# Performance work log

Hardware: AMD Instinct MI355X
Metric: run time of the kernel (lower is better)

Reference implementation:

```python
import math
import jax, jax.numpy as jnp
import numpy as np

B, C, T, N, H = 4, 512, 2048, 4096, 4


def setup_inputs() -> dict:
    key = jax.random.key(0)
    ks = jax.random.split(key, 6)
    w = lambda k, shape: jax.random.normal(k, shape, dtype=jnp.float32) * 0.02
    return {
        "hidden_states": jax.random.normal(ks[0], (B, C, T), dtype=jnp.float32),
        "codebook_hidden_states": jax.random.normal(ks[1], (N, C), dtype=jnp.float32),
        # Linear weights stored as (in, out) so application is x @ W + b
        "Wq": w(ks[2], (C, C)), "bq": jnp.zeros((C,), jnp.float32),
        "Wk": w(ks[3], (C, C)), "bk": jnp.zeros((C,), jnp.float32),
        "Wv": w(ks[4], (C, C)), "bv": jnp.zeros((C,), jnp.float32),
        "Wp": w(ks[5], (C, H)), "bp": jnp.zeros((H,), jnp.float32),
    }


def reference(hidden_states, codebook_hidden_states, Wq, bq, Wk, bk, Wv, bv, Wp, bp):
    b, c, t = hidden_states.shape
    n = codebook_hidden_states.shape[0]
    h = bp.shape[0]
    d = c // h
    hs = hidden_states.transpose(0, 2, 1)                               # [B,T,C]
    q = (hs @ Wq + bq).reshape(b, t, h, d).transpose(0, 2, 1, 3)        # [B,H,T,d]
    k = (codebook_hidden_states @ Wk + bk).reshape(n, h, d).transpose(1, 0, 2)  # [H,N,d]
    v = codebook_hidden_states @ Wv + bv                                # [N,C]
    cg = hs @ Wp + bp                                                   # [B,T,H] head-pool gates
    scale = 1.0 / math.sqrt(d)
    logits_h = jnp.einsum('bhtd,hnd->bhnt', q, k) * scale               # [B,H,N,T]
    logits = jnp.einsum('bth,bhnt->bnt', cg, logits_h) / math.sqrt(h)   # [B,N,T]
    soft = jax.nn.softmax(logits, axis=1)                               # over codebook axis N
    idx = jnp.argmax(soft, axis=1)                                      # [B,T]
    hard = jax.nn.one_hot(idx, n, dtype=logits.dtype).transpose(0, 2, 1)  # [B,N,T]
    # straight-through: value == hard, gradient flows through soft
    one_hot = soft + jax.lax.stop_gradient(hard - soft)
    z_q = jnp.einsum('bnt,nd->bdt', one_hot, v)                         # [B,C,T]
    return logits, idx[:, None, :], z_q
```

## Files before the change

kernel.cpp:

```cpp
#include <hip/hip_runtime.h>
#include <hip/hip_bf16.h>
#include <cstddef>
#include <cstdint>

#define BB 4
#define CC 512
#define TT 2048
#define NN 4096
#define HH 4

constexpr float KFAC       = 0.04419417382415922f;
constexpr float INV_S18    = 1.0f / 262144.0f;
constexpr float INV_SCALE2 = 1.0f / (512.0f * 512.0f);

typedef _Float16 f16x8 __attribute__((ext_vector_type(8)));
typedef _Float16 f16x4 __attribute__((ext_vector_type(4)));
typedef float    f32x4 __attribute__((ext_vector_type(4)));

__device__ __forceinline__ void gld16(const void* g, void* s) {
    __builtin_amdgcn_global_load_lds(
        (const __attribute__((address_space(1))) void*)g,
        (__attribute__((address_space(3))) void*)s, 16, 0, 0);
}

struct HL { _Float16 h, l; };
__device__ __forceinline__ HL split512(float x) {
    float v = x * 512.0f;
    _Float16 h = (_Float16)v;
    return { h, (_Float16)(v - (float)h) };
}

__global__ __launch_bounds__(256) void k_split(
    const float* __restrict__ src, _Float16* __restrict__ hi, _Float16* __restrict__ lo, int n4)
{
    int q = blockIdx.x * 256 + threadIdx.x;
    if (q >= n4) return;
    float4 v = *(const float4*)(src + (size_t)q * 4);
    f16x4 H, L;
    HL a = split512(v.x); H[0] = a.h; L[0] = a.l;
    HL b = split512(v.y); H[1] = b.h; L[1] = b.l;
    HL c = split512(v.z); H[2] = c.h; L[2] = c.l;
    HL d = split512(v.w); H[3] = d.h; L[3] = d.l;
    *(f16x4*)(hi + (size_t)q * 4) = H;
    *(f16x4*)(lo + (size_t)q * 4) = L;
}

__device__ __forceinline__ void tsplit_body(
    const float* __restrict__ src, _Float16* __restrict__ hi, _Float16* __restrict__ lo,
    int S, int R, int r0, int s0)
{
    __shared__ float ls[64][65];
    const int tid = threadIdx.x;
    #pragma unroll
    for (int i = 0; i < 4; ++i) {
        int q = tid + i * 256;
        int row = q >> 4, c4 = (q & 15) * 4;
        float4 v = *(const float4*)(src + (size_t)(r0 + row) * S + s0 + c4);
        ls[row][c4] = v.x; ls[row][c4 + 1] = v.y;
        ls[row][c4 + 2] = v.z; ls[row][c4 + 3] = v.w;
    }
    __syncthreads();
    #pragma unroll
    for (int i = 0; i < 2; ++i) {
        int q = tid + i * 256;
        int orow = q >> 3, seg = (q & 7) * 8;
        f16x8 H, L;
        #pragma unroll
        for (int j = 0; j < 8; ++j) {
            HL s = split512(ls[seg + j][orow]);
            H[j] = s.h; L[j] = s.l;
        }
        size_t off = (size_t)(s0 + orow) * R + r0 + seg;
        *(f16x8*)(hi + off) = H;
        *(f16x8*)(lo + off) = L;
    }
}

__global__ __launch_bounds__(256) void k_tsplit(
    const float* __restrict__ src, _Float16* __restrict__ hi, _Float16* __restrict__ lo,
    long sbatch, long dbatch, int S, int R)
{
    src += (size_t)blockIdx.z * sbatch;
    hi  += (size_t)blockIdx.z * dbatch;
    lo  += (size_t)blockIdx.z * dbatch;
    tsplit_body(src, hi, lo, S, R, blockIdx.y * 64, blockIdx.x * 64);
}

__global__ __launch_bounds__(256) void k_tsplit_w(
    const float* __restrict__ w0, const float* __restrict__ w1, const float* __restrict__ w2,
    _Float16* __restrict__ h0, _Float16* __restrict__ h1, _Float16* __restrict__ h2,
    _Float16* __restrict__ l0, _Float16* __restrict__ l1, _Float16* __restrict__ l2)
{
    const int z = blockIdx.z;
    const float* src = z == 0 ? w0 : z == 1 ? w1 : w2;
    _Float16* hi = z == 0 ? h0 : z == 1 ? h1 : h2;
    _Float16* lo = z == 0 ? l0 : z == 1 ? l1 : l2;
    tsplit_body(src, hi, lo, CC, CC, blockIdx.y * 64, blockIdx.x * 64);
}

#define MFMA_TILE_DECLS                                                       \
    __shared__ __align__(16) _Float16 Ah[128][32];                            \
    __shared__ __align__(16) _Float16 Al[128][32];                            \
    __shared__ __align__(16) _Float16 Bh[128][32];                            \
    __shared__ __align__(16) _Float16 Bl[128][32];                            \
    const int tid  = threadIdx.x;                                             \
    const int w    = tid >> 6;                                                \
    const int l    = tid & 63;                                                \
    const int quad = l >> 4;                                                  \
    const int l15  = l & 15;                                                  \
    const int wm   = (w >> 1) * 64;                                           \
    const int wn   = (w & 1) * 64;                                            \
    const int rA   = l >> 2;                                                  \
    const int cA   = (l & 3) * 8;                                             \
    f32x4 acc[4][4];                                                          \
    _Pragma("unroll") for (int i = 0; i < 4; ++i)                             \
        _Pragma("unroll") for (int j = 0; j < 4; ++j)                         \
            acc[i][j] = (f32x4){0.f, 0.f, 0.f, 0.f};

#define MFMA_TILE_STAGE(pAh, pAl, pBh, pBl, k0, srcStride)                    \
    gld16(pAh + k0,                    &Ah[w * 32][0]);                       \
    gld16(pAh + k0 + 16 * (srcStride), &Ah[w * 32 + 16][0]);                  \
    gld16(pAl + k0,                    &Al[w * 32][0]);                       \
    gld16(pAl + k0 + 16 * (srcStride), &Al[w * 32 + 16][0]);                  \
    gld16(pBh + k0,                    &Bh[w * 32][0]);                       \
    gld16(pBh + k0 + 16 * (srcStride), &Bh[w * 32 + 16][0]);                  \
    gld16(pBl + k0,                    &Bl[w * 32][0]);                       \
    gld16(pBl + k0 + 16 * (srcStride), &Bl[w * 32 + 16][0]);

#define MFMA_TILE_COMPUTE                                                     \
    {                                                                         \
        f16x8 fah[4], fal[4], fbh[4], fbl[4];                                 \
        _Pragma("unroll") for (int i = 0; i < 4; ++i) {                       \
            fah[i] = *(const f16x8*)&Ah[wm + i * 16 + l15][quad * 8];         \
            fal[i] = *(const f16x8*)&Al[wm + i * 16 + l15][quad * 8];         \
            fbh[i] = *(const f16x8*)&Bh[wn + i * 16 + l15][quad * 8];         \
            fbl[i] = *(const f16x8*)&Bl[wn + i * 16 + l15][quad * 8];         \
        }                                                                     \
        _Pragma("unroll") for (int i = 0; i < 4; ++i)                         \
            _Pragma("unroll") for (int j = 0; j < 4; ++j) {                   \
                acc[i][j] = __builtin_amdgcn_mfma_f32_16x16x32_f16(fah[i], fbh[j], acc[i][j], 0, 0, 0); \
                acc[i][j] = __builtin_amdgcn_mfma_f32_16x16x32_f16(fah[i], fbl[j], acc[i][j], 0, 0, 0); \
                acc[i][j] = __builtin_amdgcn_mfma_f32_16x16x32_f16(fal[i], fbh[j], acc[i][j], 0, 0, 0); \
            }                                                                 \
    }

__global__ __launch_bounds__(256, 2) void k_proj_all(
    const _Float16* __restrict__ hsTh, const _Float16* __restrict__ hsTl,
    const _Float16* __restrict__ cbhi, const _Float16* __restrict__ cblo,
    const _Float16* __restrict__ wqTh, const _Float16* __restrict__ wqTl,
    const _Float16* __restrict__ wkTh, const _Float16* __restrict__ wkTl,
    const _Float16* __restrict__ wvTh, const _Float16* __restrict__ wvTl,
    const float* __restrict__ bq, const float* __restrict__ bk, const float* __restrict__ bv,
    const float* __restrict__ Wp, const float* __restrict__ bp,
    _Float16* __restrict__ qhi, _Float16* __restrict__ qlo,
    _Float16* __restrict__ khi, _Float16* __restrict__ klo, float* __restrict__ vproj)
{
    const int z    = blockIdx.z;
    const int y    = blockIdx.y;
    const int c0   = blockIdx.x * 128;
    const int path = z == 0 ? 0 : (y < 32 ? 1 : 2);
    const int m0   = (z == 0 ? y : (y & 31)) * 128;
    const int hblk = c0 >> 7;

    const _Float16* srcAh = z == 0 ? hsTh : cbhi;
    const _Float16* srcAl = z == 0 ? hsTl : cblo;
    const _Float16* bTh   = path == 0 ? wqTh : path == 1 ? wkTh : wvTh;
    const _Float16* bTl   = path == 0 ? wqTl : path == 1 ? wkTl : wvTl;
    const float*    bias  = path == 0 ? bq   : path == 1 ? bk   : bv;

    MFMA_TILE_DECLS
    __shared__ float wp_sh[32];
    __shared__ float gate_sh[128];
    float gate = 0.f;

    const _Float16* pAh = srcAh + (size_t)(m0 + w * 32 + rA) * CC + cA;
    const _Float16* pAl = srcAl + (size_t)(m0 + w * 32 + rA) * CC + cA;
    const _Float16* pBh = bTh   + (size_t)(c0 + w * 32 + rA) * CC + cA;
    const _Float16* pBl = bTl   + (size_t)(c0 + w * 32 + rA) * CC + cA;

    for (int k0 = 0; k0 < CC; k0 += 32) {
        MFMA_TILE_STAGE(pAh, pAl, pBh, pBl, k0, CC)
        if (path == 0 && tid < 32) wp_sh[tid] = Wp[(size_t)(k0 + tid) * HH + hblk];
        __syncthreads();
        MFMA_TILE_COMPUTE
        if (path == 0 && tid < 128) {
            #pragma unroll
            for (int s = 0; s < 4; ++s) {
                f16x8 hv = *(const f16x8*)&Ah[tid][s * 8];
                f16x8 lv = *(const f16x8*)&Al[tid][s * 8];
                #pragma unroll
                for (int jj = 0; jj < 8; ++jj)
                    gate = fmaf((float)hv[jj] + (float)lv[jj], wp_sh[s * 8 + jj], gate);
            }
        }
        __syncthreads();
    }

    if (path == 0) {
        if (tid < 128)
            gate_sh[tid] = (gate * (1.0f / 512.0f) + bp[hblk]) * KFAC;
        __syncthreads();
        #pragma unroll
        for (int i = 0; i < 4; ++i)
            #pragma unroll
            for (int j = 0; j < 4; ++j) {
                int col = c0 + wn + j * 16 + l15;
                float bi = bias[col];
                #pragma unroll
                for (int r = 0; r < 4; ++r) {
                    int rloc = wm + i * 16 + quad * 4 + r;
                    float v = fmaf(acc[i][j][r], INV_S18, bi) * gate_sh[rloc];
                    HL s = split512(v);
                    qhi[(size_t)(m0 + rloc) * CC + col] = s.h;
                    qlo[(size_t)(m0 + rloc) * CC + col] = s.l;
                }
            }
    } else if (path == 1) {
        #pragma unroll
        for (int i = 0; i < 4; ++i)
            #pragma unroll
            for (int j = 0; j < 4; ++j) {
                int col = c0 + wn + j * 16 + l15;
                float bi = bias[col];
                #pragma unroll
                for (int r = 0; r < 4; ++r) {
                    int row = m0 + wm + i * 16 + quad * 4 + r;
                    float v = fmaf(acc[i][j][r], INV_S18, bi);
                    HL s = split512(v);
                    khi[(size_t)row * CC + col] = s.h;
                    klo[(size_t)row * CC + col] = s.l;
                }
            }
    } else {
        #pragma unroll
        for (int i = 0; i < 4; ++i)
            #pragma unroll
            for (int j = 0; j < 4; ++j) {
                int col = c0 + wn + j * 16 + l15;
                float bi = bias[col];
                #pragma unroll
                for (int r = 0; r < 4; ++r) {
                    int row = m0 + wm + i * 16 + quad * 4 + r;
                    vproj[(size_t)row * CC + col] = fmaf(acc[i][j][r], INV_S18, bi);
                }
            }
    }
}

#define BAR   __builtin_amdgcn_s_barrier()
#define LGKM0 { asm volatile("s_waitcnt lgkmcnt(0)" ::: "memory"); __builtin_amdgcn_sched_barrier(0); }
#define PRIO1 __builtin_amdgcn_s_setprio(1)
#define PRIO0 __builtin_amdgcn_s_setprio(0)

#define STAGE_A(D, KT) {                                                      \
    int sg_ = (KT) >> 3; int kof_ = ((KT) & 7) * 64;                          \
    const _Float16* ab_ = (sg_ == 1 ? klo : khi) + arow0 + kof_;              \
    gld16(ab_ + soff0,         &smem[(D) * 32768 + (w * 2 + 0) * 512]);       \
    gld16(ab_ + soff1,         &smem[(D) * 32768 + (w * 2 + 1) * 512]);       \
    gld16(ab_ + 65536 + soff0, &smem[(D) * 32768 + 8192 + (w * 2 + 0) * 512]);\
    gld16(ab_ + 65536 + soff1, &smem[(D) * 32768 + 8192 + (w * 2 + 1) * 512]);\
}
#define STAGE_B(D, KT) {                                                      \
    int sg_ = (KT) >> 3; int kof_ = ((KT) & 7) * 64;                          \
    const _Float16* bb_ = (sg_ == 2 ? qlo : qhi) + brow0 + kof_;              \
    gld16(bb_ + soff0,         &smem[(D) * 32768 + 16384 + (w * 2 + 0) * 512]);\
    gld16(bb_ + soff1,         &smem[(D) * 32768 + 16384 + (w * 2 + 1) * 512]);\
    gld16(bb_ + 65536 + soff0, &smem[(D) * 32768 + 24576 + (w * 2 + 0) * 512]);\
    gld16(bb_ + 65536 + soff1, &smem[(D) * 32768 + 24576 + (w * 2 + 1) * 512]);\
}
#define RD_A(D, HF) {                                                         \
    _Pragma("unroll") for (int ii = 0; ii < 4; ++ii)                          \
      _Pragma("unroll") for (int kk = 0; kk < 2; ++kk)                        \
        ah[ii][kk] = *(const f16x8*)&smem[(D) * 32768 + ha * 8192 +           \
                         ((HF) * 4 + ii) * 1024 + kk * 32 + rdoffh];          \
}
#define RD_B(D, HF) {                                                         \
    _Pragma("unroll") for (int jj = 0; jj < 2; ++jj)                          \
      _Pragma("unroll") for (int kk = 0; kk < 2; ++kk)                        \
        bf[(HF) * 2 + jj][kk] = *(const f16x8*)&smem[(D) * 32768 + 16384 +    \
            hb * 8192 + wb64f + ((HF) * 2 + jj) * 1024 + kk * 32 + rdoffh];   \
}
#define MM(AH, BH) {                                                          \
    _Pragma("unroll") for (int kk = 0; kk < 2; ++kk)                          \
      _Pragma("unroll") for (int ii = 0; ii < 4; ++ii)                        \
        _Pragma("unroll") for (int jj = 0; jj < 2; ++jj)                      \
          acc[(AH) * 4 + ii][(BH) * 2 + jj] =                                 \
            __builtin_amdgcn_mfma_f32_16x16x32_f16(ah[ii][kk],                \
                bf[(BH) * 2 + jj][kk], acc[(AH) * 4 + ii][(BH) * 2 + jj], 0, 0, 0); \
}
#define KTILE(D, KTN, DOSTAGE) {                                              \
    if (DOSTAGE) STAGE_A(1 - (D), KTN);                                       \
    RD_A(D, 0); RD_B(D, 0);                                                   \
    BAR; LGKM0; PRIO1; MM(0, 0); PRIO0; BAR;                                  \
    if (DOSTAGE) STAGE_B(1 - (D), KTN);                                       \
    RD_B(D, 1);                                                               \
    BAR; LGKM0; PRIO1; MM(0, 1); PRIO0; BAR;                                  \
    RD_A(D, 1);                                                               \
    BAR; LGKM0; PRIO1; MM(1, 1); PRIO0; BAR;                                  \
    PRIO1; MM(1, 0); PRIO0;                                                   \
    if (DOSTAGE) { asm volatile("s_waitcnt vmcnt(0)" ::: "memory"); }         \
    BAR;                                                                      \
}

__global__ __launch_bounds__(512, 2) void k_logits_8p(
    const _Float16* __restrict__ khi, const _Float16* __restrict__ klo,
    const _Float16* __restrict__ qhi, const _Float16* __restrict__ qlo,
    float* __restrict__ logits,
    float* __restrict__ pval,
    int*   __restrict__ pidx)
{
    __shared__ __align__(16) _Float16 smem[65536];

    const int f  = blockIdx.x + 8 * (blockIdx.y + 16 * blockIdx.z);
    const int fs = (f & 7) * 64 + (f >> 3);
    const int t0 = (fs & 7) * 256;
    const int by = (fs >> 3) & 15;
    const int b  = fs >> 7;
    const int n0 = by * 256;

    const int tid  = threadIdx.x;
    const int w    = tid >> 6;
    const int l    = tid & 63;
    const int quad = l >> 4;
    const int l15  = l & 15;
    const int wm   = (w >> 2) * 128;
    const int ha   = w >> 2;
    const int wn   = (w & 3) * 64;
    const int hb   = (w & 3) >> 1;
    const int wb64f = (w & 1) * 4096;

    const size_t arow0 = (size_t)n0 * CC;
    const size_t brow0 = ((size_t)b * TT + t0) * CC;

    size_t soff0, soff1;
    {
        int p0 = (w * 2 + 0) * 64 + l;
        int s0 = p0 ^ (((p0 >> 5) & 1) << 1);
        soff0 = (size_t)(s0 >> 3) * CC + (size_t)(s0 & 7) * 8;
        int p1 = (w * 2 + 1) * 64 + l;
        int s1 = p1 ^ (((p1 >> 5) & 1) << 1);
        soff1 = (size_t)(s1 >> 3) * CC + (size_t)(s1 & 7) * 8;
    }
    const int rdoffh = (l15 * 64 + quad * 8) ^ ((((l15 >> 2) & 1)) << 4);

    f32x4 acc[8][4];
    #pragma unroll
    for (int i = 0; i < 8; ++i)
        #pragma unroll
        for (int j = 0; j < 4; ++j)
            acc[i][j] = (f32x4){0.f, 0.f, 0.f, 0.f};
    f16x8 ah[4][2];
    f16x8 bf[4][2];

    STAGE_A(0, 0); STAGE_B(0, 0);
    asm volatile("s_waitcnt vmcnt(0)" ::: "memory");
    BAR;

    for (int kt2 = 0; kt2 < 12; ++kt2) {
        const int kt = kt2 * 2;
        KTILE(0, kt + 1, 1);
        KTILE(1, kt + 2, kt2 < 11);
    }

    {
        const size_t lb = ((size_t)b * NN + n0 + wm) * TT + t0 + wn;
        #pragma unroll
        for (int i = 0; i < 8; ++i)
            #pragma unroll
            for (int r = 0; r < 4; ++r) {
                const size_t rowoff = lb + (size_t)(i * 16 + quad * 4 + r) * TT;
                #pragma unroll
                for (int j = 0; j < 4; ++j)
                    logits[rowoff + j * 16 + l15] = acc[i][j][r] * INV_SCALE2;
            }
    }
    float bvj[4]; int bnj[4];
    #pragma unroll
    for (int j = 0; j < 4; ++j) {
        float bv = -3.0e38f; int bn = 0;
        #pragma unroll
        for (int i = 0; i < 8; ++i)
            #pragma unroll
            for (int r = 0; r < 4; ++r) {
                float v = acc[i][j][r] * INV_SCALE2;
                int row = n0 + wm + i * 16 + quad * 4 + r;
                if (v > bv) { bv = v; bn = row; }
            }
        #pragma unroll
        for (int m = 16; m <= 32; m <<= 1) {
            float ov = __shfl_xor(bv, m, 64);
            int   on = __shfl_xor(bn, m, 64);
            if (ov > bv || (ov == bv && on < bn)) { bv = ov; bn = on; }
        }
        bvj[j] = bv; bnj[j] = bn;
    }
    float* rv = (float*)smem;
    int*   ri = (int*)(smem + 1024);
    __syncthreads();
    if (w >= 4 && l < 16) {
        #pragma unroll
        for (int j = 0; j < 4; ++j) {
            rv[wn + j * 16 + l] = bvj[j];
            ri[wn + j * 16 + l] = bnj[j];
        }
    }
    __syncthreads();
    if (w < 4 && l < 16) {
        #pragma unroll
        for (int j = 0; j < 4; ++j) {
            int cl = wn + j * 16 + l;
            float bv = bvj[j]; int bn = bnj[j];
            float ov = rv[cl];
            if (ov > bv) { bv = ov; bn = ri[cl]; }
            size_t o = ((size_t)b * 16 + by) * TT + t0 + cl;
            pval[o] = bv;
            pidx[o] = bn;
        }
    }
}

__global__ __launch_bounds__(256) void k_finalize(
    const float* __restrict__ pval,
    const int*   __restrict__ pidx,
    const float* __restrict__ vproj,
    float* __restrict__ idx_out,
    float* __restrict__ zq)
{
    const int b  = blockIdx.y;
    const int t0 = blockIdx.x * 32;
    const int tid = threadIdx.x;

    __shared__ int sfin[32];
    if (tid < 32) {
        const int t = t0 + tid;
        float bv = -3.0e38f; int bn = 0;
        #pragma unroll
        for (int k = 0; k < 16; ++k) {
            size_t o = ((size_t)b * 16 + k) * TT + t;
            float v = pval[o];
            if (v > bv) { bv = v; bn = pidx[o]; }
        }
        idx_out[(size_t)b * TT + t] = (float)bn;
        sfin[tid] = bn;
    }
    __syncthreads();
    for (int pos = tid; pos < 32 * CC; pos += 256) {
        int c = pos >> 5, tl = pos & 31;
        zq[((size_t)b * CC + c) * TT + t0 + tl] = vproj[(size_t)sfin[tl] * CC + c];
    }
}

extern "C" void kernel_launch(void* const* d_in, const int* in_sizes, int n_in,
                              void* d_out, int out_size, void* d_ws, size_t ws_size,
                              hipStream_t stream)
{
    (void)in_sizes; (void)n_in; (void)out_size; (void)ws_size;
    const float* hs = (const float*)d_in[0];
    const float* cb = (const float*)d_in[1];
    const float* Wq = (const float*)d_in[2];
    const float* bq = (const float*)d_in[3];
    const float* Wk = (const float*)d_in[4];
    const float* bk = (const float*)d_in[5];
    const float* Wv = (const float*)d_in[6];
    const float* bv = (const float*)d_in[7];
    const float* Wp = (const float*)d_in[8];
    const float* bp = (const float*)d_in[9];

    char* ws = (char*)d_ws;
    const size_t MB = 1024 * 1024;
    _Float16* hsTh = (_Float16*)(ws);
    _Float16* hsTl = (_Float16*)(ws + 8  * MB);
    _Float16* qhi  = (_Float16*)(ws + 16 * MB);
    _Float16* qlo  = (_Float16*)(ws + 24 * MB);
    _Float16* cbhi = (_Float16*)(ws + 32 * MB);
    _Float16* cblo = (_Float16*)(ws + 36 * MB);
    _Float16* khi  = (_Float16*)(ws + 40 * MB);
    _Float16* klo  = (_Float16*)(ws + 44 * MB);
    float*    vproj= (float*)   (ws + 48 * MB);
    _Float16* wqTh = (_Float16*)(ws + 56 * MB);
    _Float16* wqTl = (_Float16*)(ws + 56 * MB + 524288);
    _Float16* wkTh = (_Float16*)(ws + 57 * MB);
    _Float16* wkTl = (_Float16*)(ws + 57 * MB + 524288);
    _Float16* wvTh = (_Float16*)(ws + 58 * MB);
    _Float16* wvTl = (_Float16*)(ws + 58 * MB + 524288);
    float* pval = (float*)(ws + 32 * MB);
    int*   pidx = (int*)  (ws + 33 * MB);

    float* logits = (float*)d_out;
    float* idxf   = logits + (size_t)BB * NN * TT;
    float* zq     = idxf + (size_t)BB * TT;

    k_split<<<dim3((NN * CC / 4 + 255) / 256), 256, 0, stream>>>(
        cb, cbhi, cblo, NN * CC / 4);
    k_tsplit<<<dim3(TT / 64, CC / 64, BB), 256, 0, stream>>>(
        hs, hsTh, hsTl, (long)CC * TT, (long)TT * CC, TT, CC);
    k_tsplit_w<<<dim3(CC / 64, CC / 64, 3), 256, 0, stream>>>(
        Wq, Wk, Wv, wqTh, wkTh, wvTh, wqTl, wkTl, wvTl);

    k_proj_all<<<dim3(CC / 128, 64, 2), 256, 0, stream>>>(
        hsTh, hsTl, cbhi, cblo,
        wqTh, wqTl, wkTh, wkTl, wvTh, wvTl,
        bq, bk, bv, Wp, bp,
        qhi, qlo, khi, klo, vproj);

    k_logits_8p<<<dim3(TT / 256, NN / 256, BB), 512, 0, stream>>>(
        khi, klo, qhi, qlo, logits, pval, pidx);

    k_finalize<<<dim3(TT / 32, BB), 256, 0, stream>>>(
        pval, pidx, vproj, idxf, zq);
}
```

Measured before the change: 331.5 us.

## Split global-to-LDS staging into half-tiles with partial vmcnt waits

Reworks the software pipeline of the split-fp16 logits GEMM. Each next-tile load is now issued as four half-tile chunks spread across the MFMA phases, and partial vmcnt waits replace the single full drain at the end of each k-tile. The epilogue tile is peeled into its own macro. The LDS swizzle also changes to an XOR on 8-element chunks per row, which alters the read offsets. The goal is to keep more global loads in flight during compute and avoid a full memory stall per tile. The cost is tighter wait counting that must be exactly right for the data to be correct.

```diff
diff --git a/kernel.cpp b/kernel.cpp
--- a/kernel.cpp
+++ b/kernel.cpp
@@ -251,34 +251,42 @@
 #define LGKM0 { asm volatile("s_waitcnt lgkmcnt(0)" ::: "memory"); __builtin_amdgcn_sched_barrier(0); }
 #define PRIO1 __builtin_amdgcn_s_setprio(1)
 #define PRIO0 __builtin_amdgcn_s_setprio(0)
-
-#define STAGE_A(D, KT) {                                                      \
-    int sg_ = (KT) >> 3; int kof_ = ((KT) & 7) * 64;                          \
-    const _Float16* ab_ = (sg_ == 1 ? klo : khi) + arow0 + kof_;              \
-    gld16(ab_ + soff0,         &smem[(D) * 32768 + (w * 2 + 0) * 512]);       \
-    gld16(ab_ + soff1,         &smem[(D) * 32768 + (w * 2 + 1) * 512]);       \
-    gld16(ab_ + 65536 + soff0, &smem[(D) * 32768 + 8192 + (w * 2 + 0) * 512]);\
-    gld16(ab_ + 65536 + soff1, &smem[(D) * 32768 + 8192 + (w * 2 + 1) * 512]);\
-}
-#define STAGE_B(D, KT) {                                                      \
-    int sg_ = (KT) >> 3; int kof_ = ((KT) & 7) * 64;                          \
-    const _Float16* bb_ = (sg_ == 2 ? qlo : qhi) + brow0 + kof_;              \
-    gld16(bb_ + soff0,         &smem[(D) * 32768 + 16384 + (w * 2 + 0) * 512]);\
-    gld16(bb_ + soff1,         &smem[(D) * 32768 + 16384 + (w * 2 + 1) * 512]);\
-    gld16(bb_ + 65536 + soff0, &smem[(D) * 32768 + 24576 + (w * 2 + 0) * 512]);\
-    gld16(bb_ + 65536 + soff1, &smem[(D) * 32768 + 24576 + (w * 2 + 1) * 512]);\
+#define VMW(N) asm volatile("s_waitcnt vmcnt(" #N ")" ::: "memory")
+
+#define ST_A(D, HF, SRC) {                                                    \
+    _Pragma("unroll") for (int qi_ = 0; qi_ < 2; ++qi_) {                     \
+        int q_  = w * 2 + qi_;                                                \
+        int hf_ = q_ >> 3;                                                    \
+        int R0_ = (q_ & 7) * 8;                                               \
+        gld16((SRC) + (size_t)(hf_ * 128 + (HF) * 64 + R0_) * CC + lsrc,      \
+              &smem[(D) * 32768 + hf_ * 8192 + ((HF) * 64 + R0_) * 64]);      \
+    }                                                                         \
+}
+#define ST_B(D, HF, SRC) {                                                    \
+    _Pragma("unroll") for (int qi_ = 0; qi_ < 2; ++qi_) {                     \
+        int q_  = w * 2 + qi_;                                                \
+        int s_  = q_ >> 2;                                                    \
+        int R0_ = (q_ & 3) * 8;                                               \
+        int tr_ = s_ * 64 + (HF) * 32 + R0_;                                  \
+        gld16((SRC) + (size_t)tr_ * CC + lsrc,                                \
+              &smem[(D) * 32768 + 16384 + (tr_ >> 7) * 8192 + (tr_ & 127) * 64]); \
+    }                                                                         \
 }
 #define RD_A(D, HF) {                                                         \
-    _Pragma("unroll") for (int ii = 0; ii < 4; ++ii)                          \
-      _Pragma("unroll") for (int kk = 0; kk < 2; ++kk)                        \
-        ah[ii][kk] = *(const f16x8*)&smem[(D) * 32768 + ha * 8192 +           \
-                         ((HF) * 4 + ii) * 1024 + kk * 32 + rdoffh];          \
+    _Pragma("unroll") for (int ii = 0; ii < 4; ++ii) {                        \
+        ah[ii][0] = *(const f16x8*)&smem[(D) * 32768 + ha * 8192 +            \
+                        ((HF) * 4 + ii) * 1024 + rdk0];                       \
+        ah[ii][1] = *(const f16x8*)&smem[(D) * 32768 + ha * 8192 +            \
+                        ((HF) * 4 + ii) * 1024 + rdk1];                       \
+    }                                                                         \
 }
 #define RD_B(D, HF) {                                                         \
-    _Pragma("unroll") for (int jj = 0; jj < 2; ++jj)                          \
-      _Pragma("unroll") for (int kk = 0; kk < 2; ++kk)                        \
-        bf[(HF) * 2 + jj][kk] = *(const f16x8*)&smem[(D) * 32768 + 16384 +    \
-            hb * 8192 + wb64f + ((HF) * 2 + jj) * 1024 + kk * 32 + rdoffh];   \
+    _Pragma("unroll") for (int jj = 0; jj < 2; ++jj) {                        \
+        bf[(HF) * 2 + jj][0] = *(const f16x8*)&smem[(D) * 32768 + 16384 +     \
+            hb * 8192 + wb64f + ((HF) * 2 + jj) * 1024 + rdk0];               \
+        bf[(HF) * 2 + jj][1] = *(const f16x8*)&smem[(D) * 32768 + 16384 +     \
+            hb * 8192 + wb64f + ((HF) * 2 + jj) * 1024 + rdk1];               \
+    }                                                                         \
 }
 #define MM(AH, BH) {                                                          \
     _Pragma("unroll") for (int kk = 0; kk < 2; ++kk)                          \
@@ -288,18 +296,27 @@
             __builtin_amdgcn_mfma_f32_16x16x32_f16(ah[ii][kk],                \
                 bf[(BH) * 2 + jj][kk], acc[(AH) * 4 + ii][(BH) * 2 + jj], 0, 0, 0); \
 }
-#define KTILE(D, KTN, DOSTAGE) {                                              \
-    if (DOSTAGE) STAGE_A(1 - (D), KTN);                                       \
+#define KTILE(D, AN, BN) {                                                    \
+    ST_A(1 - (D), 0, AN);                                                     \
     RD_A(D, 0); RD_B(D, 0);                                                   \
-    BAR; LGKM0; PRIO1; MM(0, 0); PRIO0; BAR;                                  \
-    if (DOSTAGE) STAGE_B(1 - (D), KTN);                                       \
+    BAR; LGKM0; PRIO1; MM(0, 0); PRIO0; VMW(4); BAR;                          \
+    ST_B(1 - (D), 0, BN);                                                     \
     RD_B(D, 1);                                                               \
-    BAR; LGKM0; PRIO1; MM(0, 1); PRIO0; BAR;                                  \
+    BAR; LGKM0; PRIO1; MM(0, 1); PRIO0; VMW(4); BAR;                          \
+    ST_B(1 - (D), 1, BN);                                                     \
+    RD_A(D, 1);                                                               \
+    BAR; LGKM0; PRIO1; MM(1, 1); PRIO0; BAR;                                  \
+    ST_A(1 - (D), 1, AN);                                                     \
+    PRIO1; MM(1, 0); PRIO0; VMW(4); BAR;                                      \
+}
+#define KTILE_LAST(D) {                                                       \
+    RD_A(D, 0); RD_B(D, 0);                                                   \
+    BAR; LGKM0; PRIO1; MM(0, 0); PRIO0; VMW(2); BAR;                          \
+    RD_B(D, 1);                                                               \
+    BAR; LGKM0; PRIO1; MM(0, 1); PRIO0; VMW(0); BAR;                          \
     RD_A(D, 1);                                                               \
     BAR; LGKM0; PRIO1; MM(1, 1); PRIO0; BAR;                                  \
     PRIO1; MM(1, 0); PRIO0;                                                   \
-    if (DOSTAGE) { asm volatile("s_waitcnt vmcnt(0)" ::: "memory"); }         \
-    BAR;                                                                      \
 }
 
 __global__ __launch_bounds__(512, 2) void k_logits_8p(
@@ -332,16 +349,13 @@
     const size_t arow0 = (size_t)n0 * CC;
     const size_t brow0 = ((size_t)b * TT + t0) * CC;
 
-    size_t soff0, soff1;
-    {
-        int p0 = (w * 2 + 0) * 64 + l;
-        int s0 = p0 ^ (((p0 >> 5) & 1) << 1);
-        soff0 = (size_t)(s0 >> 3) * CC + (size_t)(s0 & 7) * 8;
-        int p1 = (w * 2 + 1) * 64 + l;
-        int s1 = p1 ^ (((p1 >> 5) & 1) << 1);
-        soff1 = (size_t)(s1 >> 3) * CC + (size_t)(s1 & 7) * 8;
-    }
-    const int rdoffh = (l15 * 64 + quad * 8) ^ ((((l15 >> 2) & 1)) << 4);
+    const int    lrow = l >> 3;
+    const int    lchk = (l & 7) ^ lrow;
+    const size_t lsrc = (size_t)lrow * CC + (size_t)lchk * 8;
+
+    const int cs0  = quad ^ (l15 & 7);
+    const int rdk0 = l15 * 64 + cs0 * 8;
+    const int rdk1 = l15 * 64 + (cs0 ^ 4) * 8;
 
     f32x4 acc[8][4];
     #pragma unroll
@@ -352,15 +366,34 @@
     f16x8 ah[4][2];
     f16x8 bf[4][2];
 
-    STAGE_A(0, 0); STAGE_B(0, 0);
-    asm volatile("s_waitcnt vmcnt(0)" ::: "memory");
-    BAR;
-
-    for (int kt2 = 0; kt2 < 12; ++kt2) {
-        const int kt = kt2 * 2;
-        KTILE(0, kt + 1, 1);
-        KTILE(1, kt + 2, kt2 < 11);
-    }
+    {
+        const _Float16* a0_ = khi + arow0;
+        const _Float16* b0_ = qhi + brow0;
+        ST_A(0, 0, a0_); ST_B(0, 0, b0_); ST_B(0, 1, b0_); ST_A(0, 1, a0_);
+    }
+    VMW(4); BAR;
+
+    #pragma unroll 1
+    for (int kt2 = 0; kt2 < 11; ++kt2) {
+        {
+            int ktn = kt2 * 2 + 1;
+            const _Float16* an = (ktn >= 8 && ktn < 16 ? klo : khi) + arow0 + (ktn & 7) * 64;
+            const _Float16* bn = (ktn >= 16 ? qlo : qhi) + brow0 + (ktn & 7) * 64;
+            KTILE(0, an, bn);
+        }
+        {
+            int ktn = kt2 * 2 + 2;
+            const _Float16* an = (ktn >= 8 && ktn < 16 ? klo : khi) + arow0 + (ktn & 7) * 64;
+            const _Float16* bn = (ktn >= 16 ? qlo : qhi) + brow0 + (ktn & 7) * 64;
+            KTILE(1, an, bn);
+        }
+    }
+    {
+        const _Float16* an = khi + arow0 + 7 * 64;
+        const _Float16* bn = qlo + brow0 + 7 * 64;
+        KTILE(0, an, bn);
+    }
+    KTILE_LAST(1);
 
     {
         const size_t lb = ((size_t)b * NN + n0 + wm) * TT + t0 + wn;
```

Result: no change. 336.6 us (+1.5%).

## Restructure logits GEMM into four-buffer K=32 pipeline with deeper prefetch

Applied to the files above, without the earlier changes.

Replaces the double-buffered K=64 tile loop with a four-stage ring of K=32 LDS tiles, keeping three tiles in flight and using partial vmcnt waits instead of draining all loads each tile. The LDS swizzle and read offsets are recomputed for the narrower tiles. The goal is to hide global-to-LDS latency behind MFMA work. The cost is more barriers per unit of K and a more complex prologue and epilogue.

```diff
diff --git a/kernel.cpp b/kernel.cpp
--- a/kernel.cpp
+++ b/kernel.cpp
@@ -251,56 +251,40 @@
 #define LGKM0 { asm volatile("s_waitcnt lgkmcnt(0)" ::: "memory"); __builtin_amdgcn_sched_barrier(0); }
 #define PRIO1 __builtin_amdgcn_s_setprio(1)
 #define PRIO0 __builtin_amdgcn_s_setprio(0)
-
-#define STAGE_A(D, KT) {                                                      \
-    int sg_ = (KT) >> 3; int kof_ = ((KT) & 7) * 64;                          \
-    const _Float16* ab_ = (sg_ == 1 ? klo : khi) + arow0 + kof_;              \
-    gld16(ab_ + soff0,         &smem[(D) * 32768 + (w * 2 + 0) * 512]);       \
-    gld16(ab_ + soff1,         &smem[(D) * 32768 + (w * 2 + 1) * 512]);       \
-    gld16(ab_ + 65536 + soff0, &smem[(D) * 32768 + 8192 + (w * 2 + 0) * 512]);\
-    gld16(ab_ + 65536 + soff1, &smem[(D) * 32768 + 8192 + (w * 2 + 1) * 512]);\
-}
-#define STAGE_B(D, KT) {                                                      \
-    int sg_ = (KT) >> 3; int kof_ = ((KT) & 7) * 64;                          \
-    const _Float16* bb_ = (sg_ == 2 ? qlo : qhi) + brow0 + kof_;              \
-    gld16(bb_ + soff0,         &smem[(D) * 32768 + 16384 + (w * 2 + 0) * 512]);\
-    gld16(bb_ + soff1,         &smem[(D) * 32768 + 16384 + (w * 2 + 1) * 512]);\
-    gld16(bb_ + 65536 + soff0, &smem[(D) * 32768 + 24576 + (w * 2 + 0) * 512]);\
-    gld16(bb_ + 65536 + soff1, &smem[(D) * 32768 + 24576 + (w * 2 + 1) * 512]);\
-}
-#define RD_A(D, HF) {                                                         \
+#define VMW(N) asm volatile("s_waitcnt vmcnt(" #N ")" ::: "memory")
+
+#define ST_A3(BUF, SRC) {                                                     \
+    gld16((SRC) + lsrc,           &smem[(BUF) * 16384 + w * 512]);            \
+    gld16((SRC) + lsrc + 64 * CC, &smem[(BUF) * 16384 + 4096 + w * 512]);     \
+}
+#define ST_B3(BUF, SRC) {                                                     \
+    gld16((SRC) + lsrc,           &smem[(BUF) * 16384 + 8192 + w * 512]);     \
+    gld16((SRC) + lsrc + 64 * CC, &smem[(BUF) * 16384 + 12288 + w * 512]);    \
+}
+#define RD_A3(BUF, H) {                                                       \
     _Pragma("unroll") for (int ii = 0; ii < 4; ++ii)                          \
-      _Pragma("unroll") for (int kk = 0; kk < 2; ++kk)                        \
-        ah[ii][kk] = *(const f16x8*)&smem[(D) * 32768 + ha * 8192 +           \
-                         ((HF) * 4 + ii) * 1024 + kk * 32 + rdoffh];          \
-}
-#define RD_B(D, HF) {                                                         \
-    _Pragma("unroll") for (int jj = 0; jj < 2; ++jj)                          \
-      _Pragma("unroll") for (int kk = 0; kk < 2; ++kk)                        \
-        bf[(HF) * 2 + jj][kk] = *(const f16x8*)&smem[(D) * 32768 + 16384 +    \
-            hb * 8192 + wb64f + ((HF) * 2 + jj) * 1024 + kk * 32 + rdoffh];   \
-}
-#define MM(AH, BH) {                                                          \
-    _Pragma("unroll") for (int kk = 0; kk < 2; ++kk)                          \
-      _Pragma("unroll") for (int ii = 0; ii < 4; ++ii)                        \
-        _Pragma("unroll") for (int jj = 0; jj < 2; ++jj)                      \
-          acc[(AH) * 4 + ii][(BH) * 2 + jj] =                                 \
-            __builtin_amdgcn_mfma_f32_16x16x32_f16(ah[ii][kk],                \
-                bf[(BH) * 2 + jj][kk], acc[(AH) * 4 + ii][(BH) * 2 + jj], 0, 0, 0); \
-}
-#define KTILE(D, KTN, DOSTAGE) {                                              \
-    if (DOSTAGE) STAGE_A(1 - (D), KTN);                                       \
-    RD_A(D, 0); RD_B(D, 0);                                                   \
-    BAR; LGKM0; PRIO1; MM(0, 0); PRIO0; BAR;                                  \
-    if (DOSTAGE) STAGE_B(1 - (D), KTN);                                       \
-    RD_B(D, 1);                                                               \
-    BAR; LGKM0; PRIO1; MM(0, 1); PRIO0; BAR;                                  \
-    RD_A(D, 1);                                                               \
-    BAR; LGKM0; PRIO1; MM(1, 1); PRIO0; BAR;                                  \
-    PRIO1; MM(1, 0); PRIO0;                                                   \
-    if (DOSTAGE) { asm volatile("s_waitcnt vmcnt(0)" ::: "memory"); }         \
-    BAR;                                                                      \
-}
+        ah[ii] = *(const f16x8*)&smem[(BUF) * 16384 + ((H) * 4 + ii) * 1024 + baseRdA]; \
+}
+#define RD_B3(BUF) {                                                          \
+    _Pragma("unroll") for (int jj = 0; jj < 4; ++jj)                          \
+        bf[jj] = *(const f16x8*)&smem[(BUF) * 16384 + baseRdB + jj * 1024];   \
+}
+#define MM3(IOFF) {                                                           \
+    _Pragma("unroll") for (int ii = 0; ii < 4; ++ii)                          \
+        _Pragma("unroll") for (int jj = 0; jj < 4; ++jj)                      \
+            acc[(IOFF) + ii][jj] = __builtin_amdgcn_mfma_f32_16x16x32_f16(    \
+                ah[ii], bf[jj], acc[(IOFF) + ii][jj], 0, 0, 0);               \
+}
+#define TILE3(BUF, SBUF, AS, BS, DOST, VW) {                                  \
+    if (DOST) ST_A3(SBUF, AS);                                                \
+    RD_A3(BUF, 0); RD_B3(BUF);                                                \
+    BAR; LGKM0; PRIO1; MM3(0); PRIO0; BAR;                                    \
+    if (DOST) ST_B3(SBUF, BS);                                                \
+    RD_A3(BUF, 1);                                                            \
+    BAR; LGKM0; PRIO1; MM3(4); PRIO0; VW; BAR;                                \
+}
+#define APTR(n) ((((n) >> 4) == 1 ? klo : khi) + arow0 + ((n) & 15) * 32)
+#define BPTR(n) ((((n) >> 4) == 2 ? qlo : qhi) + brow0 + ((n) & 15) * 32)
 
 __global__ __launch_bounds__(512, 2) void k_logits_8p(
     const _Float16* __restrict__ khi, const _Float16* __restrict__ klo,
@@ -326,22 +310,18 @@
     const int wm   = (w >> 2) * 128;
     const int ha   = w >> 2;
     const int wn   = (w & 3) * 64;
-    const int hb   = (w & 3) >> 1;
-    const int wb64f = (w & 1) * 4096;
 
     const size_t arow0 = (size_t)n0 * CC;
     const size_t brow0 = ((size_t)b * TT + t0) * CC;
 
-    size_t soff0, soff1;
-    {
-        int p0 = (w * 2 + 0) * 64 + l;
-        int s0 = p0 ^ (((p0 >> 5) & 1) << 1);
-        soff0 = (size_t)(s0 >> 3) * CC + (size_t)(s0 & 7) * 8;
-        int p1 = (w * 2 + 1) * 64 + l;
-        int s1 = p1 ^ (((p1 >> 5) & 1) << 1);
-        soff1 = (size_t)(s1 >> 3) * CC + (size_t)(s1 & 7) * 8;
-    }
-    const int rdoffh = (l15 * 64 + quad * 8) ^ ((((l15 >> 2) & 1)) << 4);
+    const int    lclog = (l & 7) ^ ((l >> 3) & 7);
+    const size_t lsrc  = (size_t)(w * 8 + (l >> 3) + (lclog >> 2) * 128) * CC
+                       + (size_t)(lclog & 3) * 8;
+
+    const int cpxA    = ((ha << 2) | quad) ^ (l15 & 7);
+    const int baseRdA = l15 * 64 + cpxA * 8;
+    const int cpxB    = ((((w & 3) >> 1) << 2) | quad) ^ (l15 & 7);
+    const int baseRdB = 8192 + (w & 1) * 4096 + l15 * 64 + cpxB * 8;
 
     f32x4 acc[8][4];
     #pragma unroll
@@ -349,18 +329,31 @@
         #pragma unroll
         for (int j = 0; j < 4; ++j)
             acc[i][j] = (f32x4){0.f, 0.f, 0.f, 0.f};
-    f16x8 ah[4][2];
-    f16x8 bf[4][2];
-
-    STAGE_A(0, 0); STAGE_B(0, 0);
-    asm volatile("s_waitcnt vmcnt(0)" ::: "memory");
-    BAR;
-
-    for (int kt2 = 0; kt2 < 12; ++kt2) {
-        const int kt = kt2 * 2;
-        KTILE(0, kt + 1, 1);
-        KTILE(1, kt + 2, kt2 < 11);
-    }
+    f16x8 ah[4];
+    f16x8 bf[4];
+
+    ST_A3(0, APTR(0)); ST_B3(0, BPTR(0));
+    ST_A3(1, APTR(1)); ST_B3(1, BPTR(1));
+    ST_A3(2, APTR(2)); ST_B3(2, BPTR(2));
+    VMW(8); BAR;
+
+    #pragma unroll 1
+    for (int g = 0; g < 11; ++g) {
+        const int kt = g * 4;
+        { const int n_ = kt + 3; const _Float16* as_ = APTR(n_); const _Float16* bs_ = BPTR(n_);
+          TILE3(0, 3, as_, bs_, 1, VMW(8)); }
+        { const int n_ = kt + 4; const _Float16* as_ = APTR(n_); const _Float16* bs_ = BPTR(n_);
+          TILE3(1, 0, as_, bs_, 1, VMW(8)); }
+        { const int n_ = kt + 5; const _Float16* as_ = APTR(n_); const _Float16* bs_ = BPTR(n_);
+          TILE3(2, 1, as_, bs_, 1, VMW(8)); }
+        { const int n_ = kt + 6; const _Float16* as_ = APTR(n_); const _Float16* bs_ = BPTR(n_);
+          TILE3(3, 2, as_, bs_, 1, VMW(8)); }
+    }
+    { const _Float16* as_ = APTR(47); const _Float16* bs_ = BPTR(47);
+      TILE3(0, 3, as_, bs_, 1, VMW(8)); }
+    TILE3(1, 0, khi, khi, 0, VMW(4));
+    TILE3(2, 0, khi, khi, 0, VMW(0));
+    TILE3(3, 0, khi, khi, 0, (void)0);
 
     {
         const size_t lb = ((size_t)b * NN + n0 + wm) * TT + t0 + wn;
```

New measurement: 335.8 us. No clear change (+1.3%).
